# Kernel optimization log

Measured on AMD Instinct MI355X. Metric: run time of the kernel, lower is better.

## Reference

```python
import jax, jax.numpy as jnp
import numpy as np

B, N, K, D, H = 32, 4096, 8, 256, 512
ITERS = 3
LN_EPS = 1e-5  # torch LayerNorm default; self.eps is unused in forward


def _ln(x, g, b):
    m = jnp.mean(x, axis=-1, keepdims=True)
    v = jnp.mean(jnp.square(x - m), axis=-1, keepdims=True)
    return (x - m) * jax.lax.rsqrt(v + LN_EPS) * g + b


def setup_inputs() -> dict:
    key = jax.random.key(0)
    ks = jax.random.split(key, 16)
    s = 0.02
    return {
        "inputs": jax.random.normal(ks[0], (B, N, D), jnp.float32),
        "slots_init": jax.random.normal(ks[1], (B, K, D), jnp.float32),
        "ln_in_g": jnp.ones((D,), jnp.float32), "ln_in_b": jnp.zeros((D,), jnp.float32),
        "ln_s_g": jnp.ones((D,), jnp.float32), "ln_s_b": jnp.zeros((D,), jnp.float32),
        "ln_ff_g": jnp.ones((D,), jnp.float32), "ln_ff_b": jnp.zeros((D,), jnp.float32),
        "Wk": s * jax.random.normal(ks[2], (D, D), jnp.float32), "bk": jnp.zeros((D,), jnp.float32),
        "Wq": s * jax.random.normal(ks[3], (D, D), jnp.float32), "bq": jnp.zeros((D,), jnp.float32),
        "Wv": s * jax.random.normal(ks[4], (D, D), jnp.float32), "bv": jnp.zeros((D,), jnp.float32),
        "W_ih": s * jax.random.normal(ks[5], (3 * D, D), jnp.float32),
        "b_ih": jnp.zeros((3 * D,), jnp.float32),
        "W_hh": s * jax.random.normal(ks[6], (3 * D, D), jnp.float32),
        "b_hh": jnp.zeros((3 * D,), jnp.float32),
        "W1": s * jax.random.normal(ks[7], (H, D), jnp.float32), "b1": jnp.zeros((H,), jnp.float32),
        "W2": s * jax.random.normal(ks[8], (D, H), jnp.float32), "b2": jnp.zeros((D,), jnp.float32),
    }


def _gru_cell(x, h, W_ih, b_ih, W_hh, b_hh):
    # PyTorch GRUCell: gates in order r, z, n
    gi = x @ W_ih.T + b_ih  # [*, 3D]
    gh = h @ W_hh.T + b_hh
    ir, iz, inn = jnp.split(gi, 3, axis=-1)
    hr, hz, hn = jnp.split(gh, 3, axis=-1)
    r = jax.nn.sigmoid(ir + hr)
    z = jax.nn.sigmoid(iz + hz)
    n = jnp.tanh(inn + r * hn)
    return (1.0 - z) * n + z * h


def reference(inputs, slots_init, ln_in_g, ln_in_b, ln_s_g, ln_s_b, ln_ff_g, ln_ff_b,
              Wk, bk, Wq, bq, Wv, bv, W_ih, b_ih, W_hh, b_hh, W1, b1, W2, b2):
    d = inputs.shape[-1]
    x = _ln(inputs, ln_in_g, ln_in_b)  # [B,N,D]
    # k, v depend only on x; hoisted out of the loop (same math as source)
    k = x @ Wk.T + bk                  # project_inputs
    v = x @ Wv.T + bv                  # project_v
    scale = 1.0 / jnp.sqrt(jnp.asarray(d, inputs.dtype))
    slots = slots_init
    for _ in range(ITERS):
        slots_prev = slots
        q = _ln(slots, ln_s_g, ln_s_b) @ Wq.T + bq          # [B,K,D]
        attn_logits = jnp.einsum('bkd,bnd->bkn', q, k) * scale
        # competitive softmax over the SLOT axis (dim=1), not keys
        attn = jax.nn.softmax(attn_logits, axis=1)          # [B,K,N]
        updates = jnp.einsum('bkn,bnd->bkd', attn, v)
        slots = _gru_cell(updates, slots_prev, W_ih, b_ih, W_hh, b_hh)
        hdd = jax.nn.relu(_ln(slots, ln_ff_g, ln_ff_b) @ W1.T + b1)
        slots = slots + hdd @ W2.T + b2
    return slots
```

## Files before the change

### kernel.cpp

```cpp
#include <hip/hip_runtime.h>
#include <hip/hip_bf16.h>
#include <cstddef>
#include <cstdint>

#define BB 32
#define NN 4096
#define KK 8
#define DD 256
#define HH 512
#define LN_EPS 1e-5f
#define SCALE 0.0625f
#define NCHUNK 32

__device__ __forceinline__ float wave_sum(float v) {
#pragma unroll
  for (int off = 32; off >= 1; off >>= 1) v += __shfl_xor(v, off);
  return v;
}

__device__ __forceinline__ float sigmoidf_(float x) { return 1.0f / (1.0f + __expf(-x)); }

__device__ __forceinline__ uint pk2bf(float x, float y) {
  __hip_bfloat16 hx = __float2bfloat16(x), hy = __float2bfloat16(y);
  return (uint)*(ushort*)&hx | ((uint)*(ushort*)&hy << 16);
}

#define OFF_G   0
#define OFF_W1  393216
#define OFF_W2  524288
#define OFF_WV  655360
#define OFF_WQ  720896
#define OFF_WK  786432
#define WB_ELEMS 851968

#define G_PRE (BB * KK)
#define G_W2B (512 * 11)
#define G_SETUP (G_PRE + G_W2B + 1)

__device__ __forceinline__ float dotp4(uint2 w, float4 s) {
  return __uint_as_float(w.x << 16) * s.x + __uint_as_float(w.x & 0xffff0000u) * s.y +
         __uint_as_float(w.y << 16) * s.z + __uint_as_float(w.y & 0xffff0000u) * s.w;
}

template <int OUT, int KL>
__device__ __forceinline__ float gemv_p(const ushort* __restrict__ wt, int j, int kb,
                                        const float* __restrict__ src) {
  const uint2* p = (const uint2*)(wt + ((size_t)(kb >> 2) * OUT + j) * 4);
  float a = 0.0f;
#pragma unroll 16
  for (int e = 0; e < KL / 4; ++e) {
    uint2 w = p[(size_t)e * OUT];
    float4 s = *(const float4*)(src + kb + e * 4);
    a += dotp4(w, s);
  }
  return a;
}

__global__ __launch_bounds__(256) void k_setup(
    const float* __restrict__ Wih, const float* __restrict__ Whh,
    const float* __restrict__ W1, const float* __restrict__ W2,
    const float* __restrict__ Wv, const float* __restrict__ Wq,
    const float* __restrict__ Wk, ushort* __restrict__ wb,
    const float* __restrict__ slots, const float* __restrict__ gs, const float* __restrict__ bs,
    const float* __restrict__ bq, const float* __restrict__ bk,
    const float* __restrict__ gi, const float* __restrict__ bi,
    const float* __restrict__ bv, float* __restrict__ bvw,
    float* __restrict__ qk, float* __restrict__ qb) {
  int blk = blockIdx.x;
  if (blk < G_PRE) {
    int row = blk;
    int t = threadIdx.x;
    int wid = t >> 6, lane = t & 63;
    __shared__ float lns[DD];
    __shared__ float qs[DD];
    __shared__ float rb[8];
    float sv = slots[(size_t)row * DD + t];
    float s = wave_sum(sv);
    float s2 = wave_sum(sv * sv);
    if (lane == 0) { rb[wid] = s; rb[4 + wid] = s2; }
    __syncthreads();
    float tot = rb[0] + rb[1] + rb[2] + rb[3];
    float tot2 = rb[4] + rb[5] + rb[6] + rb[7];
    float m = tot * (1.0f / DD);
    float var = tot2 * (1.0f / DD) - m * m;
    float rs = rsqrtf(var + LN_EPS);
    lns[t] = (sv - m) * rs * gs[t] + bs[t];
    __syncthreads();
    float acc = 0.0f;
    const float4* wr = (const float4*)(Wq + (size_t)t * DD);
#pragma unroll 4
    for (int e4 = 0; e4 < DD / 4; ++e4) {
      float4 w = wr[e4];
      float4 l = ((const float4*)lns)[e4];
      acc += w.x * l.x + w.y * l.y + w.z * l.z + w.w * l.w;
    }
    qs[t] = acc + bq[t];
    __syncthreads();
    float a2 = 0.0f;
    for (int d = 0; d < DD; ++d) a2 = fmaf(qs[d], Wk[(size_t)d * DD + t], a2);
    float a2S = SCALE * a2;
    qk[(size_t)row * DD + t] = a2S * gi[t];
    float pb = wave_sum(qs[t] * bk[t]);
    float pb2 = wave_sum(a2S * bi[t]);
    __syncthreads();
    if (lane == 0) { rb[wid] = pb; rb[4 + wid] = pb2; }
    __syncthreads();
    if (t == 0) qb[row] = SCALE * (rb[0] + rb[1] + rb[2] + rb[3]) + rb[4] + rb[5] + rb[6] + rb[7];
  } else if (blk < G_PRE + G_W2B) {
    int q2 = blk - G_PRE;
    int m = q2 >> 9;
    int idx = (q2 & 511) * 256 + threadIdx.x;
    const int sizes[11] = {65536, 65536, 65536, 65536, 65536, 65536, 131072, 131072, 65536, 65536, 65536};
    const int offs[11] = {OFF_G, OFF_G + 65536, OFF_G + 131072, OFF_G + 196608, OFF_G + 262144,
                          OFF_G + 327680, OFF_W1, OFF_W2, OFF_WV, OFF_WQ, OFF_WK};
    if (idx >= sizes[m]) return;
    int K = (m == 7) ? 512 : 256;
    int OUT = (m == 6) ? 512 : 256;
    int k = idx % K, j = idx / K;
    float v;
    switch (m) {
      case 0: case 1: case 2: v = Wih[((size_t)(m * 256 + j)) * 256 + k]; break;
      case 3: case 4: case 5: v = Whh[((size_t)((m - 3) * 256 + j)) * 256 + k]; break;
      case 6: v = W1[(size_t)j * 256 + k]; break;
      case 7: v = W2[(size_t)j * 512 + k]; break;
      case 8: v = Wv[(size_t)j * 256 + k] * gi[k]; break;
      case 9: v = Wq[(size_t)j * 256 + k]; break;
      default: v = Wk[(size_t)k * 256 + j]; break;
    }
    __hip_bfloat16 h = __float2bfloat16(v);
    wb[(size_t)offs[m] + (size_t)(k >> 2) * OUT * 4 + j * 4 + (k & 3)] = *(ushort*)&h;
  } else {
    int t = threadIdx.x;
    float a = bv[t];
    const float4* wr = (const float4*)(Wv + (size_t)t * DD);
    const float4* bb = (const float4*)bi;
#pragma unroll 4
    for (int e4 = 0; e4 < DD / 4; ++e4) {
      float4 w = wr[e4];
      float4 x = bb[e4];
      a += w.x * x.x + w.y * x.y + w.z * x.z + w.w * x.w;
    }
    bvw[t] = a;
  }
}

template <int DO_LN>
__global__ __launch_bounds__(256, 2) void k_attn_t(const ushort* __restrict__ xb_in,
                                                   ushort* __restrict__ xb_out,
                                                   const float* __restrict__ inp,
                                                   const float* __restrict__ qk,
                                                   const float* __restrict__ qb,
                                                   float* __restrict__ uxp,
                                                   float* __restrict__ sap) {
  typedef __attribute__((ext_vector_type(8))) short short8;
  typedef __attribute__((ext_vector_type(4))) float f32x4;
  union V16 { uint4 u; short8 s; ushort us[8]; };

  __shared__ __align__(16) ushort q_l[16 * 256];
  __shared__ __align__(16) ushort xt[4][32 * 256];

  int t = threadIdx.x, wid = t >> 6, lane = t & 63;
  int bI = blockIdx.x >> 5, c = blockIdx.x & 31;
  int lm = lane & 15, g = lane >> 4;
  ushort* xw = xt[wid];
  char* xwB = (char*)xw;
  char* qB = (char*)q_l;

  {
    const float* qkb = qk + (size_t)bI * (KK * DD);
    int p = t >> 3, e7 = t & 7;
#pragma unroll 1
    for (int s = 0; s < 8; ++s) {
      float qv = qkb[s * 256 + t];
      __hip_bfloat16 hb = __float2bfloat16(qv);
      float lo = qv - __bfloat162float(hb);
      __hip_bfloat16 lb = __float2bfloat16(lo);
      *(ushort*)(qB + s * 512 + (((p + s) & 31) << 4) + e7 * 2) = *(ushort*)&hb;
      *(ushort*)(qB + (s + 8) * 512 + (((p + s + 8) & 31) << 4) + e7 * 2) = *(ushort*)&lb;
    }
  }
  float qbv = qb[bI * 8 + (lane & 7)];

  int row0 = c * 128 + wid * 32;

  if (DO_LN) {
    __syncthreads();
    int q8 = lane & 7, lr = lane >> 3;
    const float* rp0 = inp + ((size_t)bI * NN + row0 + lr) * DD + q8 * 4;
    int pb = q8 >> 1, hb8 = (q8 & 1) * 8;
#pragma unroll 1
    for (int p = 0; p < 4; ++p) {
      float4 cur[8];
#pragma unroll
      for (int i = 0; i < 8; ++i) cur[i] = *(const float4*)(rp0 + (size_t)p * 8 * DD + i * 32);
      float s1 = 0.0f, s2 = 0.0f;
#pragma unroll
      for (int i = 0; i < 8; ++i) {
        s1 += cur[i].x + cur[i].y + cur[i].z + cur[i].w;
        s2 += cur[i].x * cur[i].x + cur[i].y * cur[i].y + cur[i].z * cur[i].z + cur[i].w * cur[i].w;
      }
      s1 += __shfl_xor(s1, 1); s2 += __shfl_xor(s2, 1);
      s1 += __shfl_xor(s1, 2); s2 += __shfl_xor(s2, 2);
      s1 += __shfl_xor(s1, 4); s2 += __shfl_xor(s2, 4);
      float m = s1 * (1.0f / DD);
      float var = s2 * (1.0f / DD) - m * m;
      float rs = rsqrtf(var + LN_EPS);
      int rr = p * 8 + lr;
#pragma unroll
      for (int i = 0; i < 8; ++i) {
        uint2 wv;
        wv.x = pk2bf((cur[i].x - m) * rs, (cur[i].y - m) * rs);
        wv.y = pk2bf((cur[i].z - m) * rs, (cur[i].w - m) * rs);
        *(uint2*)(xwB + ((4 * i + pb) << 9) + (rr << 4) + hb8) = wv;
      }
    }
    ushort* xbt = xb_out + ((size_t)bI * NN + row0) * DD;
#pragma unroll 1
    for (int i = 0; i < 16; ++i) {
      uint4 v = *(const uint4*)&xw[i * 512 + lane * 8];
      *(uint4*)&xbt[i * 512 + lane * 8] = v;
    }
  } else {
    const ushort* srcb = xb_in + ((size_t)bI * NN + row0) * DD;
#pragma unroll
    for (int i = 0; i < 16; ++i) {
      __builtin_amdgcn_global_load_lds(
          (__attribute__((address_space(1))) void*)(srcb + i * 512 + lane * 8),
          (__attribute__((address_space(3))) void*)&xw[i * 512], 16, 0, 0);
    }
    __builtin_amdgcn_sched_barrier(0);
    asm volatile("s_waitcnt lgkmcnt(0)\n\ts_barrier" ::: "memory");
    __builtin_amdgcn_sched_barrier(0);
  }

  int rA = lm, rB = lm + 16;
  f32x4 ac0 = {}, ac1 = {};
#pragma unroll
  for (int kk = 0; kk < 8; ++kk) {
    if (!DO_LN) {
      asm volatile("s_waitcnt vmcnt(%0)" ::"i"(14 - 2 * kk) : "memory");
    }
    V16 qf, x0, x1;
    int ch = kk * 4 + g;
    qf.u = *(const uint4*)(qB + (lm << 9) + (((ch + lm) & 31) << 4));
    x0.u = *(const uint4*)(xwB + (ch << 9) + (rA << 4));
    x1.u = *(const uint4*)(xwB + (ch << 9) + (rB << 4));
    ac0 = __builtin_amdgcn_mfma_f32_16x16x32_bf16(x0.s, qf.s, ac0, 0, 0, 0);
    ac1 = __builtin_amdgcn_mfma_f32_16x16x32_bf16(x1.s, qf.s, ac1, 0, 0, 0);
  }

  float a0[4], a1[4];
  {
    float lv0[4], lv1[4], mx0[4], mx1[4], ss0[4], ss1[4];
#pragma unroll
    for (int r = 0; r < 4; ++r) {
      lv0[r] = ac0[r] + __shfl_xor(ac0[r], 8) + qbv;
      lv1[r] = ac1[r] + __shfl_xor(ac1[r], 8) + qbv;
      mx0[r] = lv0[r]; mx1[r] = lv1[r];
    }
#pragma unroll
    for (int off = 1; off <= 4; off <<= 1) {
#pragma unroll
      for (int r = 0; r < 4; ++r) {
        mx0[r] = fmaxf(mx0[r], __shfl_xor(mx0[r], off));
        mx1[r] = fmaxf(mx1[r], __shfl_xor(mx1[r], off));
      }
    }
#pragma unroll
    for (int r = 0; r < 4; ++r) {
      a0[r] = __expf(lv0[r] - mx0[r]);
      a1[r] = __expf(lv1[r] - mx1[r]);
      ss0[r] = a0[r]; ss1[r] = a1[r];
    }
#pragma unroll
    for (int off = 1; off <= 4; off <<= 1) {
#pragma unroll
      for (int r = 0; r < 4; ++r) {
        ss0[r] += __shfl_xor(ss0[r], off);
        ss1[r] += __shfl_xor(ss1[r], off);
      }
    }
#pragma unroll
    for (int r = 0; r < 4; ++r) {
      a0[r] *= __frcp_rn(ss0[r]);
      a1[r] *= __frcp_rn(ss1[r]);
    }
  }
  float sacc = 0.0f;
#pragma unroll
  for (int r = 0; r < 4; ++r) sacc += a0[r] + a1[r];
  sacc += __shfl_xor(sacc, 16);
  sacc += __shfl_xor(sacc, 32);

  bool lop = (lane & 8) != 0;
  V16 au;
  {
    float t8[8];
#pragma unroll
    for (int e = 0; e < 8; ++e) {
      float av = (e < 4) ? a0[e] : a1[e - 4];
      if (lop) {
        __hip_bfloat16 hb = __float2bfloat16(av);
        av = av - __bfloat162float(hb);
      }
      t8[e] = av;
    }
    au.u = make_uint4(pk2bf(t8[0], t8[1]), pk2bf(t8[2], t8[3]),
                      pk2bf(t8[4], t8[5]), pk2bf(t8[6], t8[7]));
  }

  f32x4 av4[16];
#pragma unroll
  for (int i = 0; i < 16; ++i) av4[i] = (f32x4){0.0f, 0.0f, 0.0f, 0.0f};
#pragma unroll
  for (int dc = 0; dc < 16; ++dc) {
    int d = dc * 16 + lm, dch = d >> 3, d7b = (d & 7) * 2;
    int r0 = 4 * g, r2 = 16 + 4 * g;
    const char* pl = xwB + (dch << 9) + d7b;
    V16 bu;
    bu.u.x = (uint)*(const ushort*)(pl + ((r0 + 0) << 4)) |
             ((uint)*(const ushort*)(pl + ((r0 + 1) << 4)) << 16);
    bu.u.y = (uint)*(const ushort*)(pl + ((r0 + 2) << 4)) |
             ((uint)*(const ushort*)(pl + ((r0 + 3) << 4)) << 16);
    bu.u.z = (uint)*(const ushort*)(pl + ((r2 + 0) << 4)) |
             ((uint)*(const ushort*)(pl + ((r2 + 1) << 4)) << 16);
    bu.u.w = (uint)*(const ushort*)(pl + ((r2 + 2) << 4)) |
             ((uint)*(const ushort*)(pl + ((r2 + 3) << 4)) << 16);
    av4[dc] = __builtin_amdgcn_mfma_f32_16x16x32_bf16(au.s, bu.s, av4[dc], 0, 0, 0);
  }

  float* uxwf = (float*)xw;
#pragma unroll
  for (int dc = 0; dc < 16; ++dc) {
#pragma unroll
    for (int r = 0; r < 4; ++r) {
      float v = av4[dc][r];
      float o = v + __shfl_xor(v, 32);
      if (lane < 32) uxwf[(g * 4 + r) * 256 + dc * 16 + lm] = o;
    }
  }
  __syncthreads();
  float* sredf = (float*)q_l;
  if (lane < 8) sredf[wid * 8 + lane] = sacc;
  __syncthreads();
  {
    const float* x0f = (const float*)xt[0];
    const float* x1f = (const float*)xt[1];
    const float* x2f = (const float*)xt[2];
    const float* x3f = (const float*)xt[3];
    size_t obase = ((size_t)(bI * NCHUNK + c)) * (KK * DD);
#pragma unroll 1
    for (int u = 0; u < 8; ++u) {
      int idx = u * 256 + t;
      uxp[obase + idx] = x0f[idx] + x1f[idx] + x2f[idx] + x3f[idx];
    }
    if (t < 8)
      sap[((size_t)(bI * NCHUNK + c)) * KK + t] =
          sredf[t] + sredf[8 + t] + sredf[16 + t] + sredf[24 + t];
  }
}

__global__ __launch_bounds__(1024) void k_fused(const float* __restrict__ slots_in,
                                                const float* __restrict__ uxp,
                                                const float* __restrict__ sap,
                                                const ushort* __restrict__ wb,
                                                const float* __restrict__ bv,
                                                const float* __restrict__ bih, const float* __restrict__ bhh,
                                                const float* __restrict__ gff, const float* __restrict__ bff,
                                                const float* __restrict__ b1, const float* __restrict__ b2,
                                                const float* __restrict__ gs, const float* __restrict__ bs,
                                                const float* __restrict__ bq, const float* __restrict__ bk,
                                                const float* __restrict__ gi, const float* __restrict__ bi,
                                                float* __restrict__ dst,
                                                float* __restrict__ qk_out,
                                                float* __restrict__ qb_out,
                                                int last) {
  const ushort* WG = wb + OFF_G;
  const ushort* W1p = wb + OFF_W1;
  const ushort* W2p = wb + OFF_W2;
  const ushort* WVp = wb + OFF_WV;
  const ushort* WQp = wb + OFF_WQ;
  const ushort* WKp = wb + OFF_WK;

  __shared__ float ux_s[DD], h_s[DD], upd_s[DD], hn_s[DD], ln_s[DD];
  __shared__ float g_s[6][DD];
  __shared__ float hdd_s[HH];
  __shared__ float tmp4_s[4][DD];
  __shared__ float red_s[16];
  __shared__ float sA_s;
  float* tmpH = &tmp4_s[0][0];

  int t = threadIdx.x, d = t & 255, qr = t >> 8;
  int wid = t >> 6, lane = t & 63;
  int r = blockIdx.x, b = r >> 3, k = r & 7;

  {
    const float* p = uxp + (((size_t)(b * NCHUNK + qr * 8)) * KK + k) * DD + d;
    float s = 0.0f;
#pragma unroll
    for (int i = 0; i < 8; ++i) s += p[(size_t)i * KK * DD];
    tmp4_s[qr][d] = s;
  }
  if (t < 256) h_s[t] = slots_in[(size_t)r * DD + t];
  if (t >= 960) {
    int c = t - 960;
    float v = (c < NCHUNK) ? sap[((size_t)(b * NCHUNK + c)) * KK + k] : 0.0f;
    v = wave_sum(v);
    if (lane == 0) sA_s = v;
  }
  __syncthreads();
  if (t < 256) ux_s[t] = tmp4_s[0][t] + tmp4_s[1][t] + tmp4_s[2][t] + tmp4_s[3][t];
  __syncthreads();

  tmp4_s[qr][d] = gemv_p<256, 64>(WVp, d, qr * 64, ux_s);
  __syncthreads();
  if (t < 256) upd_s[t] = tmp4_s[0][t] + tmp4_s[1][t] + tmp4_s[2][t] + tmp4_s[3][t] + bv[t] * sA_s;
  __syncthreads();

  {
    int g = qr;
    const float* src = (g < 3) ? upd_s : h_s;
    float a = gemv_p<256, 256>(WG + (size_t)g * 65536, d, 0, src);
    g_s[g][d] = a + ((g < 3) ? bih[g * 256 + d] : bhh[d]);
    if (t < 512) {
      int g2 = 4 + (t >> 8), j2 = t & 255;
      float a2 = gemv_p<256, 256>(WG + (size_t)g2 * 65536, j2, 0, h_s);
      g_s[g2][j2] = a2 + bhh[(g2 - 3) * 256 + j2];
    }
  }
  __syncthreads();
  if (t < 256) {
    float rr = sigmoidf_(g_s[0][t] + g_s[3][t]);
    float zz = sigmoidf_(g_s[1][t] + g_s[4][t]);
    float nn = tanhf(g_s[2][t] + rr * g_s[5][t]);
    hn_s[t] = (1.0f - zz) * nn + zz * h_s[t];
  }
  __syncthreads();

  if (t < 256) {
    float v = hn_s[t];
    float sm = wave_sum(v), sq = wave_sum(v * v);
    if (lane == 0) { red_s[wid] = sm; red_s[8 + wid] = sq; }
  }
  __syncthreads();
  if (t < 256) {
    float v = hn_s[t];
    float tot = red_s[0] + red_s[1] + red_s[2] + red_s[3];
    float tot2 = red_s[8] + red_s[9] + red_s[10] + red_s[11];
    float m = tot * (1.0f / DD);
    float var = tot2 * (1.0f / DD) - m * m;
    float rs = rsqrtf(var + LN_EPS);
    ln_s[t] = (v - m) * rs * gff[t] + bff[t];
  }
  __syncthreads();

  {
    int o = t & 511, kh = t >> 9;
    tmpH[kh * 512 + o] = gemv_p<512, 128>(W1p, o, kh * 128, ln_s);
  }
  __syncthreads();
  if (t < 512) hdd_s[t] = fmaxf(tmpH[t] + tmpH[512 + t] + b1[t], 0.0f);
  __syncthreads();

  tmp4_s[qr][d] = gemv_p<256, 128>(W2p, d, qr * 128, hdd_s);
  __syncthreads();
  if (t < 256) {
    float o = hn_s[t] + tmp4_s[0][t] + tmp4_s[1][t] + tmp4_s[2][t] + tmp4_s[3][t] + b2[t];
    dst[(size_t)r * DD + t] = o;
    ux_s[t] = o;
  }
  __syncthreads();

  if (!last) {
    if (t < 256) {
      float v = ux_s[t];
      float sm = wave_sum(v), sq = wave_sum(v * v);
      if (lane == 0) { red_s[wid] = sm; red_s[8 + wid] = sq; }
    }
    __syncthreads();
    if (t < 256) {
      float v = ux_s[t];
      float tot = red_s[0] + red_s[1] + red_s[2] + red_s[3];
      float tot2 = red_s[8] + red_s[9] + red_s[10] + red_s[11];
      float m = tot * (1.0f / DD);
      float var = tot2 * (1.0f / DD) - m * m;
      float rs = rsqrtf(var + LN_EPS);
      ln_s[t] = (v - m) * rs * gs[t] + bs[t];
    }
    __syncthreads();
    tmp4_s[qr][d] = gemv_p<256, 64>(WQp, d, qr * 64, ln_s);
    __syncthreads();
    if (t < 256) {
      float qv = tmp4_s[0][t] + tmp4_s[1][t] + tmp4_s[2][t] + tmp4_s[3][t] + bq[t];
      upd_s[t] = qv;
      float sb = wave_sum(qv * bk[t]);
      if (lane == 0) red_s[wid] = sb;
    }
    __syncthreads();
    {
      float a = gemv_p<256, 64>(WKp, d, qr * 64, upd_s);
      tmp4_s[qr][d] = a;
    }
    __syncthreads();
    if (t < 256) {
      float qkv = SCALE * (tmp4_s[0][t] + tmp4_s[1][t] + tmp4_s[2][t] + tmp4_s[3][t]);
      qk_out[(size_t)r * DD + t] = qkv * gi[t];
      float pb2 = wave_sum(qkv * bi[t]);
      if (lane == 0) red_s[8 + wid] = pb2;
    }
    __syncthreads();
    if (t == 0) qb_out[r] = SCALE * (red_s[0] + red_s[1] + red_s[2] + red_s[3]) +
                            red_s[8] + red_s[9] + red_s[10] + red_s[11];
  }
}

extern "C" void kernel_launch(void* const* d_in, const int* in_sizes, int n_in,
                              void* d_out, int out_size, void* d_ws, size_t ws_size,
                              hipStream_t stream) {
  const float* inputs = (const float*)d_in[0];
  const float* slots_init = (const float*)d_in[1];
  const float* ln_in_g = (const float*)d_in[2];
  const float* ln_in_b = (const float*)d_in[3];
  const float* ln_s_g = (const float*)d_in[4];
  const float* ln_s_b = (const float*)d_in[5];
  const float* ln_ff_g = (const float*)d_in[6];
  const float* ln_ff_b = (const float*)d_in[7];
  const float* Wk = (const float*)d_in[8];
  const float* bk = (const float*)d_in[9];
  const float* Wq = (const float*)d_in[10];
  const float* bq = (const float*)d_in[11];
  const float* Wv = (const float*)d_in[12];
  const float* bv = (const float*)d_in[13];
  const float* Wih = (const float*)d_in[14];
  const float* bih = (const float*)d_in[15];
  const float* Whh = (const float*)d_in[16];
  const float* bhh = (const float*)d_in[17];
  const float* W1 = (const float*)d_in[18];
  const float* b1 = (const float*)d_in[19];
  const float* W2 = (const float*)d_in[20];
  const float* b2 = (const float*)d_in[21];
  float* outp = (float*)d_out;

  char* w = (char*)d_ws;
  ushort* xb = (ushort*)w;       w += (size_t)BB * NN * DD * 2;
  float* qk = (float*)w;         w += (size_t)BB * KK * DD * 4;
  float* qb = (float*)w;         w += (size_t)BB * KK * 4;
  float* uxp = (float*)w;        w += (size_t)BB * NCHUNK * KK * DD * 4;
  float* sap = (float*)w;        w += (size_t)BB * NCHUNK * KK * 4;
  float* slots_ws = (float*)w;   w += (size_t)BB * KK * DD * 4;
  ushort* wb = (ushort*)w;       w += (size_t)WB_ELEMS * 2;
  float* bvw = (float*)w;        w += (size_t)DD * 4;

  k_setup<<<G_SETUP, 256, 0, stream>>>(Wih, Whh, W1, W2, Wv, Wq, Wk, wb,
                                       slots_init, ln_s_g, ln_s_b, bq, bk,
                                       ln_in_g, ln_in_b, bv, bvw, qk, qb);

  for (int it = 0; it < 3; ++it) {
    if (it == 0)
      k_attn_t<1><<<BB * NCHUNK, 256, 0, stream>>>(nullptr, xb, inputs, qk, qb, uxp, sap);
    else
      k_attn_t<0><<<BB * NCHUNK, 256, 0, stream>>>(xb, nullptr, nullptr, qk, qb, uxp, sap);
    const float* sin = (it == 0) ? slots_init : slots_ws;
    float* dst = (it == 2) ? outp : slots_ws;
    k_fused<<<BB * KK, 1024, 0, stream>>>(sin, uxp, sap, wb,
                                          bvw, bih, bhh, ln_ff_g, ln_ff_b, b1, b2,
                                          ln_s_g, ln_s_b, bq, bk, ln_in_g, ln_in_b,
                                          dst, qk, qb, (it == 2) ? 1 : 0);
  }
}
```

Before: 240.0 us.

## Share one row tile across waves in attention kernel and split work by D

Restructures the attention kernel so all four waves cooperate on one shared 32-row tile at a time, looping over four tiles, instead of each wave owning a private 32-row tile. The logit dot product is split across waves by feature chunk and reduced through a small LDS scratch, and the attention-times-V product is split by output column, so each wave keeps only four accumulators and writes its slice directly. This cuts LDS per block from four tiles to one and lowers register use, allowing launch bounds of four blocks per CU for higher occupancy. The trade-off is several extra block-wide barriers per tile and less independent work per wave.

```diff
diff --git a/kernel.cpp b/kernel.cpp
--- a/kernel.cpp
+++ b/kernel.cpp
@@ -145,7 +145,7 @@
 }
 
 template <int DO_LN>
-__global__ __launch_bounds__(256, 2) void k_attn_t(const ushort* __restrict__ xb_in,
+__global__ __launch_bounds__(256, 4) void k_attn_t(const ushort* __restrict__ xb_in,
                                                    ushort* __restrict__ xb_out,
                                                    const float* __restrict__ inp,
                                                    const float* __restrict__ qk,
@@ -157,13 +157,13 @@
   union V16 { uint4 u; short8 s; ushort us[8]; };
 
   __shared__ __align__(16) ushort q_l[16 * 256];
-  __shared__ __align__(16) ushort xt[4][32 * 256];
+  __shared__ __align__(16) ushort xbuf[32 * 256];
+  __shared__ __align__(16) float scr[4 * 512];
 
   int t = threadIdx.x, wid = t >> 6, lane = t & 63;
   int bI = blockIdx.x >> 5, c = blockIdx.x & 31;
   int lm = lane & 15, g = lane >> 4;
-  ushort* xw = xt[wid];
-  char* xwB = (char*)xw;
+  char* xwB = (char*)xbuf;
   char* qB = (char*)q_l;
 
   {
@@ -181,18 +181,22 @@
   }
   float qbv = qb[bI * 8 + (lane & 7)];
 
-  int row0 = c * 128 + wid * 32;
-
-  if (DO_LN) {
-    __syncthreads();
-    int q8 = lane & 7, lr = lane >> 3;
-    const float* rp0 = inp + ((size_t)bI * NN + row0 + lr) * DD + q8 * 4;
-    int pb = q8 >> 1, hb8 = (q8 & 1) * 8;
+  f32x4 avacc[4];
+#pragma unroll
+  for (int i = 0; i < 4; ++i) avacc[i] = (f32x4){0.0f, 0.0f, 0.0f, 0.0f};
+  float stot = 0.0f;
+
 #pragma unroll 1
-    for (int p = 0; p < 4; ++p) {
+  for (int tt = 0; tt < 4; ++tt) {
+    int row0 = c * 128 + tt * 32;
+
+    if (DO_LN) {
+      __syncthreads();
+      int q8 = t & 7, rr = t >> 3;
+      const float* rp = inp + ((size_t)bI * NN + row0 + rr) * DD + q8 * 4;
       float4 cur[8];
 #pragma unroll
-      for (int i = 0; i < 8; ++i) cur[i] = *(const float4*)(rp0 + (size_t)p * 8 * DD + i * 32);
+      for (int i = 0; i < 8; ++i) cur[i] = *(const float4*)(rp + i * 32);
       float s1 = 0.0f, s2 = 0.0f;
 #pragma unroll
       for (int i = 0; i < 8; ++i) {
@@ -205,7 +209,7 @@
       float m = s1 * (1.0f / DD);
       float var = s2 * (1.0f / DD) - m * m;
       float rs = rsqrtf(var + LN_EPS);
-      int rr = p * 8 + lr;
+      int pb = q8 >> 1, hb8 = (q8 & 1) * 8;
 #pragma unroll
       for (int i = 0; i < 8; ++i) {
         uint2 wv;
@@ -213,151 +217,137 @@
         wv.y = pk2bf((cur[i].z - m) * rs, (cur[i].w - m) * rs);
         *(uint2*)(xwB + ((4 * i + pb) << 9) + (rr << 4) + hb8) = wv;
       }
-    }
-    ushort* xbt = xb_out + ((size_t)bI * NN + row0) * DD;
-#pragma unroll 1
-    for (int i = 0; i < 16; ++i) {
-      uint4 v = *(const uint4*)&xw[i * 512 + lane * 8];
-      *(uint4*)&xbt[i * 512 + lane * 8] = v;
-    }
-  } else {
-    const ushort* srcb = xb_in + ((size_t)bI * NN + row0) * DD;
-#pragma unroll
-    for (int i = 0; i < 16; ++i) {
-      __builtin_amdgcn_global_load_lds(
-          (__attribute__((address_space(1))) void*)(srcb + i * 512 + lane * 8),
-          (__attribute__((address_space(3))) void*)&xw[i * 512], 16, 0, 0);
-    }
-    __builtin_amdgcn_sched_barrier(0);
-    asm volatile("s_waitcnt lgkmcnt(0)\n\ts_barrier" ::: "memory");
-    __builtin_amdgcn_sched_barrier(0);
-  }
-
-  int rA = lm, rB = lm + 16;
-  f32x4 ac0 = {}, ac1 = {};
-#pragma unroll
-  for (int kk = 0; kk < 8; ++kk) {
-    if (!DO_LN) {
-      asm volatile("s_waitcnt vmcnt(%0)" ::"i"(14 - 2 * kk) : "memory");
-    }
-    V16 qf, x0, x1;
-    int ch = kk * 4 + g;
-    qf.u = *(const uint4*)(qB + (lm << 9) + (((ch + lm) & 31) << 4));
-    x0.u = *(const uint4*)(xwB + (ch << 9) + (rA << 4));
-    x1.u = *(const uint4*)(xwB + (ch << 9) + (rB << 4));
-    ac0 = __builtin_amdgcn_mfma_f32_16x16x32_bf16(x0.s, qf.s, ac0, 0, 0, 0);
-    ac1 = __builtin_amdgcn_mfma_f32_16x16x32_bf16(x1.s, qf.s, ac1, 0, 0, 0);
-  }
-
-  float a0[4], a1[4];
-  {
-    float lv0[4], lv1[4], mx0[4], mx1[4], ss0[4], ss1[4];
+      __syncthreads();
+      ushort* xbt = xb_out + ((size_t)bI * NN + row0) * DD;
+#pragma unroll
+      for (int i = 0; i < 4; ++i)
+        *(uint4*)((char*)xbt + i * 4096 + t * 16) = *(const uint4*)(xwB + i * 4096 + t * 16);
+    } else {
+      __syncthreads();
+      const ushort* srcb = xb_in + ((size_t)bI * NN + row0) * DD;
+#pragma unroll
+      for (int i = 0; i < 4; ++i) {
+        __builtin_amdgcn_global_load_lds(
+            (__attribute__((address_space(1))) void*)(srcb + i * 2048 + wid * 512 + lane * 8),
+            (__attribute__((address_space(3))) void*)(xbuf + i * 2048 + wid * 512), 16, 0, 0);
+      }
+      asm volatile("s_waitcnt vmcnt(0)" ::: "memory");
+      __syncthreads();
+    }
+
+    f32x4 p0 = (f32x4){0.0f, 0.0f, 0.0f, 0.0f}, p1 = (f32x4){0.0f, 0.0f, 0.0f, 0.0f};
+#pragma unroll
+    for (int kx = 0; kx < 2; ++kx) {
+      int ch = (2 * wid + kx) * 4 + g;
+      V16 qf, x0, x1;
+      qf.u = *(const uint4*)(qB + (lm << 9) + (((ch + lm) & 31) << 4));
+      x0.u = *(const uint4*)(xwB + (ch << 9) + (lm << 4));
+      x1.u = *(const uint4*)(xwB + (ch << 9) + ((lm + 16) << 4));
+      p0 = __builtin_amdgcn_mfma_f32_16x16x32_bf16(x0.s, qf.s, p0, 0, 0, 0);
+      p1 = __builtin_amdgcn_mfma_f32_16x16x32_bf16(x1.s, qf.s, p1, 0, 0, 0);
+    }
+    *(f32x4*)&scr[wid * 512 + lane * 8] = p0;
+    *(f32x4*)&scr[wid * 512 + lane * 8 + 4] = p1;
+    __syncthreads();
+
+    f32x4 s0 = (f32x4){0.0f, 0.0f, 0.0f, 0.0f}, s1v = (f32x4){0.0f, 0.0f, 0.0f, 0.0f};
+#pragma unroll
+    for (int w2 = 0; w2 < 4; ++w2) {
+      s0 += *(const f32x4*)&scr[w2 * 512 + lane * 8];
+      s1v += *(const f32x4*)&scr[w2 * 512 + lane * 8 + 4];
+    }
+
+    float a0[4], a1[4];
+    {
+      float lv0[4], lv1[4], mx0[4], mx1[4], ss0[4], ss1[4];
+#pragma unroll
+      for (int r = 0; r < 4; ++r) {
+        lv0[r] = s0[r] + __shfl_xor(s0[r], 8) + qbv;
+        lv1[r] = s1v[r] + __shfl_xor(s1v[r], 8) + qbv;
+        mx0[r] = lv0[r]; mx1[r] = lv1[r];
+      }
+#pragma unroll
+      for (int off = 1; off <= 4; off <<= 1) {
+#pragma unroll
+        for (int r = 0; r < 4; ++r) {
+          mx0[r] = fmaxf(mx0[r], __shfl_xor(mx0[r], off));
+          mx1[r] = fmaxf(mx1[r], __shfl_xor(mx1[r], off));
+        }
+      }
+#pragma unroll
+      for (int r = 0; r < 4; ++r) {
+        a0[r] = __expf(lv0[r] - mx0[r]);
+        a1[r] = __expf(lv1[r] - mx1[r]);
+        ss0[r] = a0[r]; ss1[r] = a1[r];
+      }
+#pragma unroll
+      for (int off = 1; off <= 4; off <<= 1) {
+#pragma unroll
+        for (int r = 0; r < 4; ++r) {
+          ss0[r] += __shfl_xor(ss0[r], off);
+          ss1[r] += __shfl_xor(ss1[r], off);
+        }
+      }
+#pragma unroll
+      for (int r = 0; r < 4; ++r) {
+        a0[r] *= __frcp_rn(ss0[r]);
+        a1[r] *= __frcp_rn(ss1[r]);
+      }
+    }
+    float sacc = 0.0f;
+#pragma unroll
+    for (int r = 0; r < 4; ++r) sacc += a0[r] + a1[r];
+    sacc += __shfl_xor(sacc, 16);
+    sacc += __shfl_xor(sacc, 32);
+    stot += sacc;
+
+    bool lop = (lane & 8) != 0;
+    V16 au;
+    {
+      float t8[8];
+#pragma unroll
+      for (int e = 0; e < 8; ++e) {
+        float av = (e < 4) ? a0[e] : a1[e - 4];
+        if (lop) {
+          __hip_bfloat16 hb = __float2bfloat16(av);
+          av = av - __bfloat162float(hb);
+        }
+        t8[e] = av;
+      }
+      au.u = make_uint4(pk2bf(t8[0], t8[1]), pk2bf(t8[2], t8[3]),
+                        pk2bf(t8[4], t8[5]), pk2bf(t8[6], t8[7]));
+    }
+
+#pragma unroll
+    for (int cc = 0; cc < 4; ++cc) {
+      int dc = 4 * wid + cc;
+      int d = dc * 16 + lm, dch = d >> 3, d7b = (d & 7) * 2;
+      int r0 = 4 * g, r2 = 16 + 4 * g;
+      const char* pl = xwB + (dch << 9) + d7b;
+      V16 bu;
+      bu.u.x = (uint)*(const ushort*)(pl + ((r0 + 0) << 4)) |
+               ((uint)*(const ushort*)(pl + ((r0 + 1) << 4)) << 16);
+      bu.u.y = (uint)*(const ushort*)(pl + ((r0 + 2) << 4)) |
+               ((uint)*(const ushort*)(pl + ((r0 + 3) << 4)) << 16);
+      bu.u.z = (uint)*(const ushort*)(pl + ((r2 + 0) << 4)) |
+               ((uint)*(const ushort*)(pl + ((r2 + 1) << 4)) << 16);
+      bu.u.w = (uint)*(const ushort*)(pl + ((r2 + 2) << 4)) |
+               ((uint)*(const ushort*)(pl + ((r2 + 3) << 4)) << 16);
+      avacc[cc] = __builtin_amdgcn_mfma_f32_16x16x32_bf16(au.s, bu.s, avacc[cc], 0, 0, 0);
+    }
+  }
+
+  size_t obase = ((size_t)(bI * NCHUNK + c)) * (KK * DD);
+#pragma unroll
+  for (int cc = 0; cc < 4; ++cc) {
 #pragma unroll
     for (int r = 0; r < 4; ++r) {
-      lv0[r] = ac0[r] + __shfl_xor(ac0[r], 8) + qbv;
-      lv1[r] = ac1[r] + __shfl_xor(ac1[r], 8) + qbv;
-      mx0[r] = lv0[r]; mx1[r] = lv1[r];
-    }
-#pragma unroll
-    for (int off = 1; off <= 4; off <<= 1) {
-#pragma unroll
-      for (int r = 0; r < 4; ++r) {
-        mx0[r] = fmaxf(mx0[r], __shfl_xor(mx0[r], off));
-        mx1[r] = fmaxf(mx1[r], __shfl_xor(mx1[r], off));
-      }
-    }
-#pragma unroll
-    for (int r = 0; r < 4; ++r) {
-      a0[r] = __expf(lv0[r] - mx0[r]);
-      a1[r] = __expf(lv1[r] - mx1[r]);
-      ss0[r] = a0[r]; ss1[r] = a1[r];
-    }
-#pragma unroll
-    for (int off = 1; off <= 4; off <<= 1) {
-#pragma unroll
-      for (int r = 0; r < 4; ++r) {
-        ss0[r] += __shfl_xor(ss0[r], off);
-        ss1[r] += __shfl_xor(ss1[r], off);
-      }
-    }
-#pragma unroll
-    for (int r = 0; r < 4; ++r) {
-      a0[r] *= __frcp_rn(ss0[r]);
-      a1[r] *= __frcp_rn(ss1[r]);
-    }
-  }
-  float sacc = 0.0f;
-#pragma unroll
-  for (int r = 0; r < 4; ++r) sacc += a0[r] + a1[r];
-  sacc += __shfl_xor(sacc, 16);
-  sacc += __shfl_xor(sacc, 32);
-
-  bool lop = (lane & 8) != 0;
-  V16 au;
-  {
-    float t8[8];
-#pragma unroll
-    for (int e = 0; e < 8; ++e) {
-      float av = (e < 4) ? a0[e] : a1[e - 4];
-      if (lop) {
-        __hip_bfloat16 hb = __float2bfloat16(av);
-        av = av - __bfloat162float(hb);
-      }
-      t8[e] = av;
-    }
-    au.u = make_uint4(pk2bf(t8[0], t8[1]), pk2bf(t8[2], t8[3]),
-                      pk2bf(t8[4], t8[5]), pk2bf(t8[6], t8[7]));
-  }
-
-  f32x4 av4[16];
-#pragma unroll
-  for (int i = 0; i < 16; ++i) av4[i] = (f32x4){0.0f, 0.0f, 0.0f, 0.0f};
-#pragma unroll
-  for (int dc = 0; dc < 16; ++dc) {
-    int d = dc * 16 + lm, dch = d >> 3, d7b = (d & 7) * 2;
-    int r0 = 4 * g, r2 = 16 + 4 * g;
-    const char* pl = xwB + (dch << 9) + d7b;
-    V16 bu;
-    bu.u.x = (uint)*(const ushort*)(pl + ((r0 + 0) << 4)) |
-             ((uint)*(const ushort*)(pl + ((r0 + 1) << 4)) << 16);
-    bu.u.y = (uint)*(const ushort*)(pl + ((r0 + 2) << 4)) |
-             ((uint)*(const ushort*)(pl + ((r0 + 3) << 4)) << 16);
-    bu.u.z = (uint)*(const ushort*)(pl + ((r2 + 0) << 4)) |
-             ((uint)*(const ushort*)(pl + ((r2 + 1) << 4)) << 16);
-    bu.u.w = (uint)*(const ushort*)(pl + ((r2 + 2) << 4)) |
-             ((uint)*(const ushort*)(pl + ((r2 + 3) << 4)) << 16);
-    av4[dc] = __builtin_amdgcn_mfma_f32_16x16x32_bf16(au.s, bu.s, av4[dc], 0, 0, 0);
-  }
-
-  float* uxwf = (float*)xw;
-#pragma unroll
-  for (int dc = 0; dc < 16; ++dc) {
-#pragma unroll
-    for (int r = 0; r < 4; ++r) {
-      float v = av4[dc][r];
+      float v = avacc[cc][r];
       float o = v + __shfl_xor(v, 32);
-      if (lane < 32) uxwf[(g * 4 + r) * 256 + dc * 16 + lm] = o;
-    }
-  }
-  __syncthreads();
-  float* sredf = (float*)q_l;
-  if (lane < 8) sredf[wid * 8 + lane] = sacc;
-  __syncthreads();
-  {
-    const float* x0f = (const float*)xt[0];
-    const float* x1f = (const float*)xt[1];
-    const float* x2f = (const float*)xt[2];
-    const float* x3f = (const float*)xt[3];
-    size_t obase = ((size_t)(bI * NCHUNK + c)) * (KK * DD);
-#pragma unroll 1
-    for (int u = 0; u < 8; ++u) {
-      int idx = u * 256 + t;
-      uxp[obase + idx] = x0f[idx] + x1f[idx] + x2f[idx] + x3f[idx];
-    }
-    if (t < 8)
-      sap[((size_t)(bI * NCHUNK + c)) * KK + t] =
-          sredf[t] + sredf[8 + t] + sredf[16 + t] + sredf[24 + t];
-  }
+      if (lane < 32) uxp[obase + (g * 4 + r) * 256 + (4 * wid + cc) * 16 + lm] = o;
+    }
+  }
+  if (wid == 0 && lane < 8) sap[((size_t)(bI * NCHUNK + c)) * KK + lane] = stot;
 }
 
 __global__ __launch_bounds__(1024) void k_fused(const float* __restrict__ slots_in,
```

Result: faster. 230.8 us (median of 2 runs) (-3.8%).
